# Kernel tuning notes

Measured on AMD Instinct MI355X. Metric: run time of the kernel, lower is better.

## Reference

```python
import jax, jax.numpy as jnp
import numpy as np

N, E, D, H = 50000, 800000, 64, 4  # nodes, edges, dim_h, heads
NEG_SLOPE = 0.2
BN_EPS = 1e-5


def setup_inputs() -> dict:
    key = jax.random.key(0)
    ks = jax.random.split(key, 8)
    x = jax.random.normal(ks[0], (N, D), dtype=jnp.float32)
    edge_index = jax.random.randint(ks[1], (2, E), 0, N, dtype=jnp.int32)
    s = 1.0 / np.sqrt(D)
    W_lin = jax.random.normal(ks[2], (D, D), dtype=jnp.float32) * s
    b_lin = jnp.zeros((D,), dtype=jnp.float32)
    prelu_w = jnp.full((D,), 0.25, dtype=jnp.float32)
    W_gat = jax.random.normal(ks[3], (H * D, D), dtype=jnp.float32) * s  # maps D -> H*D
    att_src = jax.random.normal(ks[4], (H, D), dtype=jnp.float32) * 0.1
    att_dst = jax.random.normal(ks[5], (H, D), dtype=jnp.float32) * 0.1
    gat_bias = jnp.zeros((D,), dtype=jnp.float32)
    bn_gamma = jnp.ones((D,), dtype=jnp.float32)
    bn_beta = jnp.zeros((D,), dtype=jnp.float32)
    return dict(x=x, edge_index=edge_index, W_lin=W_lin, b_lin=b_lin,
                prelu_w=prelu_w, W_gat=W_gat, att_src=att_src, att_dst=att_dst,
                gat_bias=gat_bias, bn_gamma=bn_gamma, bn_beta=bn_beta)


def _gat_mod_fwd(x, edge_index, W_lin, b_lin, prelu_w, W_gat, att_src, att_dst,
                 gat_bias, bn_gamma, bn_beta):
    # --- pre linear + PReLU ---
    x = x @ W_lin.T + b_lin
    x = jnp.where(x >= 0, x, prelu_w * x)  # per-channel PReLU

    # --- GATConv (concat=False -> head mean), add_self_loops=True ---
    h = (x @ W_gat.T).reshape(N, H, D)              # [N,H,D]
    a_src = jnp.einsum('nhd,hd->nh', h, att_src)    # [N,H]
    a_dst = jnp.einsum('nhd,hd->nh', h, att_dst)    # [N,H]

    loop = jnp.arange(N, dtype=edge_index.dtype)
    src = jnp.concatenate([edge_index[0], loop])    # [E+N]
    dst = jnp.concatenate([edge_index[1], loop])

    e = jax.nn.leaky_relu(a_src[src] + a_dst[dst], NEG_SLOPE)   # [E+N, H]
    # segment softmax over destination nodes (self loops guarantee non-empty)
    emax = jax.ops.segment_max(e, dst, num_segments=N)          # [N,H]
    p = jnp.exp(e - emax[dst])
    denom = jax.ops.segment_sum(p, dst, num_segments=N)         # [N,H]
    alpha = p / denom[dst]                                      # [E+N,H]

    msg = h[src] * alpha[:, :, None]                            # [E+N,H,D]
    out = jax.ops.segment_sum(msg, dst, num_segments=N)         # [N,H,D]
    out = out.mean(axis=1) + gat_bias                           # [N,D]

    # --- BatchNorm1d (training: batch stats) + ReLU ---
    mean = out.mean(axis=0)
    var = out.var(axis=0)
    out = bn_gamma * (out - mean) * jax.lax.rsqrt(var + BN_EPS) + bn_beta
    return jax.nn.relu(out)


def reference(x, edge_index, W_lin, b_lin, prelu_w, W_gat, att_src, att_dst,
              gat_bias, bn_gamma, bn_beta):
    return _gat_mod_fwd(x, edge_index, W_lin, b_lin, prelu_w, W_gat, att_src,
                        att_dst, gat_bias, bn_gamma, bn_beta)
```

## Files before the change

### kernel.cpp

```cpp
#include <hip/hip_runtime.h>
#include <hip/hip_fp16.h>

#define NEG_SLOPE 0.2f
#define BN_EPS 1e-5f

constexpr int D = 64;
constexpr int H = 4;

constexpr int PSORT = 128;
constexpr int MAXW2 = 12544;

typedef _Float16 half2_t __attribute__((ext_vector_type(2)));
typedef _Float16 half4_t __attribute__((ext_vector_type(4)));
typedef _Float16 half8_t __attribute__((ext_vector_type(8)));
typedef float f32x4_t __attribute__((ext_vector_type(4)));
typedef int i32x4 __attribute__((ext_vector_type(4)));

union Rec {
    i32x4 i4;
    struct { int idx; int pad; half4_t w; } f;
};

#define MFMA16(a, b, c) __builtin_amdgcn_mfma_f32_16x16x32_f16(a, b, c, 0, 0, 0)

#if __has_builtin(__builtin_amdgcn_fdot2)
#define FDOT2(a, b, c) __builtin_amdgcn_fdot2((a), (b), (c), false)
#else
#define FDOT2(a, b, c) ((c) + (float)(a)[0] * (float)(b)[0] + (float)(a)[1] * (float)(b)[1])
#endif

__device__ inline half2_t h2cast(unsigned int u) { return __builtin_bit_cast(half2_t, u); }

__device__ inline float lrelu(float v) { return (v >= 0.f) ? v : NEG_SLOPE * v; }

__device__ inline void split8(const float* p, bool ok, half8_t& hi, half8_t& lo) {
    float f[8];
    if (ok) {
        float4 a = *(const float4*)p;
        float4 b = *(const float4*)(p + 4);
        f[0] = a.x; f[1] = a.y; f[2] = a.z; f[3] = a.w;
        f[4] = b.x; f[5] = b.y; f[6] = b.z; f[7] = b.w;
    } else {
        #pragma unroll
        for (int j = 0; j < 8; j++) f[j] = 0.f;
    }
    #pragma unroll
    for (int j = 0; j < 8; j++) {
        _Float16 h = (_Float16)f[j];
        hi[j] = h;
        lo[j] = (_Float16)(f[j] - (float)h);
    }
}

__global__ __launch_bounds__(256) void k_node(
    const float* __restrict__ x,
    const float* __restrict__ W_lin, const float* __restrict__ b_lin,
    const float* __restrict__ prelu_w, const float* __restrict__ W_gat,
    const float* __restrict__ att_src, const float* __restrict__ att_dst,
    _Float16* __restrict__ hh, float* __restrict__ asrc_ws,
    float* __restrict__ adst_ws, int N)
{
    __shared__ _Float16 smem[32 * 264];
    _Float16* __restrict__ h_lds = smem;
    _Float16* __restrict__ x1hi  = smem;
    _Float16* __restrict__ x1lo  = smem + 32 * 72;

    const int t = threadIdx.x;
    const int w = t >> 6;
    const int l = t & 63;
    const int li = l & 15;
    const int lq = l >> 4;
    const int base = blockIdx.x * 32;
    const int nvalid = min(32, N - base);

    f32x4_t accA[2] = {};
    {
        half8_t blh[2], bll[2];
        const int n = 16 * w + li;
        #pragma unroll
        for (int ks = 0; ks < 2; ks++)
            split8(W_lin + n * 64 + 32 * ks + 8 * lq, true, blh[ks], bll[ks]);
        #pragma unroll
        for (int mt = 0; mt < 2; mt++) {
            const int row = base + 16 * mt + li;
            const bool ok = row < N;
            #pragma unroll
            for (int ks = 0; ks < 2; ks++) {
                half8_t ah, al;
                split8(x + (size_t)row * 64 + 32 * ks + 8 * lq, ok, ah, al);
                accA[mt] = MFMA16(ah, blh[ks], accA[mt]);
                accA[mt] = MFMA16(al, blh[ks], accA[mt]);
                accA[mt] = MFMA16(ah, bll[ks], accA[mt]);
            }
        }
    }

    {
        const int n = 16 * w + li;
        const float bl = b_lin[n];
        const float pw = prelu_w[n];
        #pragma unroll
        for (int mt = 0; mt < 2; mt++) {
            #pragma unroll
            for (int r = 0; r < 4; r++) {
                const int m = 16 * mt + lq * 4 + r;
                float v = accA[mt][r] + bl;
                v = (v >= 0.f) ? v : pw * v;
                _Float16 hi = (_Float16)v;
                x1hi[m * 72 + n] = hi;
                x1lo[m * 72 + n] = (_Float16)(v - (float)hi);
            }
        }
    }
    __syncthreads();

    half8_t xah[2][2], xal[2][2];
    #pragma unroll
    for (int mt = 0; mt < 2; mt++) {
        #pragma unroll
        for (int ks = 0; ks < 2; ks++) {
            const int off = (16 * mt + li) * 72 + 32 * ks + 8 * lq;
            xah[mt][ks] = *(const half8_t*)(&x1hi[off]);
            xal[mt][ks] = *(const half8_t*)(&x1lo[off]);
        }
    }
    f32x4_t accB[2][4] = {};
    #pragma unroll
    for (int nt = 0; nt < 4; nt++) {
        half8_t wh[2], wl[2];
        const int c = 64 * w + 16 * nt + li;
        #pragma unroll
        for (int ks = 0; ks < 2; ks++)
            split8(W_gat + (size_t)c * 64 + 32 * ks + 8 * lq, true, wh[ks], wl[ks]);
        #pragma unroll
        for (int mt = 0; mt < 2; mt++) {
            #pragma unroll
            for (int ks = 0; ks < 2; ks++) {
                accB[mt][nt] = MFMA16(xah[mt][ks], wh[ks], accB[mt][nt]);
                accB[mt][nt] = MFMA16(xal[mt][ks], wh[ks], accB[mt][nt]);
                accB[mt][nt] = MFMA16(xah[mt][ks], wl[ks], accB[mt][nt]);
            }
        }
    }

    {
        float asv[4], adv[4];
        #pragma unroll
        for (int nt = 0; nt < 4; nt++) {
            const int c = 64 * w + 16 * nt + li;
            asv[nt] = att_src[c];
            adv[nt] = att_dst[c];
        }
        #pragma unroll
        for (int mt = 0; mt < 2; mt++) {
            #pragma unroll
            for (int r = 0; r < 4; r++) {
                float s = 0.f, dsum = 0.f;
                #pragma unroll
                for (int nt = 0; nt < 4; nt++) {
                    s += accB[mt][nt][r] * asv[nt];
                    dsum += accB[mt][nt][r] * adv[nt];
                }
                #pragma unroll
                for (int off = 1; off < 16; off <<= 1) {
                    s += __shfl_xor(s, off, 64);
                    dsum += __shfl_xor(dsum, off, 64);
                }
                if (li == 0) {
                    const int m = 16 * mt + lq * 4 + r;
                    if (m < nvalid) {
                        asrc_ws[(size_t)(base + m) * H + w] = s;
                        adst_ws[(size_t)(base + m) * H + w] = dsum;
                    }
                }
            }
        }
    }

    __syncthreads();

    #pragma unroll
    for (int mt = 0; mt < 2; mt++) {
        #pragma unroll
        for (int nt = 0; nt < 4; nt++) {
            #pragma unroll
            for (int r = 0; r < 4; r++) {
                const int m = 16 * mt + lq * 4 + r;
                const int d = 16 * nt + li;
                h_lds[m * 264 + d * 4 + w] = (_Float16)accB[mt][nt][r];
            }
        }
    }
    __syncthreads();
    {
        const int chunks = nvalid * 32;
        const uint4* src = (const uint4*)h_lds;
        uint4* dst = (uint4*)(hh + (size_t)base * 256);
        for (int i = t; i < chunks; i += 256) {
            int row = i >> 5;
            int col = i & 31;
            dst[i] = src[row * 33 + col];
        }
    }
}

__global__ __launch_bounds__(1024) void k_hist(const int* __restrict__ ei,
                                               unsigned int* __restrict__ gcnt,
                                               int E, int chunk, int N2, int WTOT) {
    __shared__ unsigned int cnt[MAXW2];
    const int p = blockIdx.x & (PSORT - 1);
    const int pass = blockIdx.x >> 7;
    const int t = threadIdx.x;
    const int W2 = N2 >> 1;
    for (int i = t; i < W2; i += 1024) cnt[i] = 0;
    __syncthreads();
    const int e0 = p * chunk;
    const int e1 = min(E, e0 + chunk);
    const int nlo = pass * N2;
    for (int e = e0 + t; e < e1; e += 1024) {
        int dl = ei[E + e] - nlo;
        if ((unsigned)dl < (unsigned)N2)
            atomicAdd(&cnt[dl >> 1], 1u << ((dl & 1) * 16));
    }
    __syncthreads();
    unsigned int* dst = gcnt + (size_t)p * WTOT + (size_t)pass * W2;
    for (int i = t; i < W2; i += 1024) dst[i] = cnt[i];
}

__global__ __launch_bounds__(256) void k_off(unsigned int* __restrict__ gcnt,
                                             int* __restrict__ gcount,
                                             int* __restrict__ offs,
                                             int* __restrict__ deg,
                                             int N, int WTOT) {
    __shared__ int sm[256];
    __shared__ int sbase;
    const int t = threadIdx.x;
    const int i = blockIdx.x * 256 + t;
    int d0 = 0, d1 = 0;
    if (i < WTOT) {
        unsigned int run = 0;
        for (int p = 0; p < PSORT; p++) {
            unsigned int* q = gcnt + (size_t)p * WTOT + i;
            unsigned int c = *q;
            *q = run;
            run += c;
        }
        d0 = (int)(run & 0xffffu);
        d1 = (int)(run >> 16);
    }
    int v = d0 + d1;
    sm[t] = v;
    __syncthreads();
    for (int off = 1; off < 256; off <<= 1) {
        int u = (t >= off) ? sm[t - off] : 0;
        __syncthreads();
        sm[t] += u;
        __syncthreads();
    }
    if (t == 255) sbase = atomicAdd(gcount, sm[255]);
    __syncthreads();
    const int base = sbase + sm[t] - v;
    const int n0 = 2 * i;
    if (n0 < N)     { offs[n0] = base;          deg[n0] = d0; }
    if (n0 + 1 < N) { offs[n0 + 1] = base + d0; deg[n0 + 1] = d1; }
}

__global__ __launch_bounds__(1024) void k_fill(const int* __restrict__ ei,
                                               const unsigned int* __restrict__ gcnt,
                                               const int* __restrict__ offs,
                                               const float* __restrict__ asrc,
                                               const float* __restrict__ adst,
                                               i32x4* __restrict__ recs,
                                               int E, int chunk, int N2, int WTOT) {
    __shared__ unsigned int cur[MAXW2];
    const int p = blockIdx.x & (PSORT - 1);
    const int pass = blockIdx.x >> 7;
    const int t = threadIdx.x;
    const int W2 = N2 >> 1;
    for (int i = t; i < W2; i += 1024) cur[i] = 0;
    __syncthreads();
    const int e0 = p * chunk;
    const int e1 = min(E, e0 + chunk);
    const int nlo = pass * N2;
    for (int e = e0 + t; e < e1; e += 1024) {
        int d = ei[E + e];
        int dl = d - nlo;
        if ((unsigned)dl >= (unsigned)N2) continue;
        int s = ei[e];
        const unsigned int sh = (unsigned)(dl & 1) * 16;
        unsigned int old = atomicAdd(&cur[dl >> 1], 1u << sh);
        int lr = (int)((old >> sh) & 0xffffu);
        int pr = (int)((gcnt[(size_t)p * WTOT + (d >> 1)] >> sh) & 0xffffu);
        int pos = offs[d] + pr + lr;
        float4 a = *(const float4*)(asrc + (size_t)s * H);
        float4 b = *(const float4*)(adst + (size_t)d * H);
        Rec r;
        r.f.idx = s;
        r.f.pad = 0;
        r.f.w[0] = (_Float16)__expf(lrelu(a.x + b.x));
        r.f.w[1] = (_Float16)__expf(lrelu(a.y + b.y));
        r.f.w[2] = (_Float16)__expf(lrelu(a.z + b.z));
        r.f.w[3] = (_Float16)__expf(lrelu(a.w + b.w));
        recs[pos] = r.i4;
    }
}

__device__ inline void edge_pair(const i32x4 ra, const i32x4 rb,
                                 const uint2 ha, const uint2 hb,
                                 float& den0, float& den1, float& den2, float& den3,
                                 float& acc0, float& acc1, float& acc2, float& acc3)
{
    const half2_t one2 = h2cast(0x3C003C00u);
    unsigned int wp0 = __builtin_amdgcn_perm((unsigned int)rb.z, (unsigned int)ra.z, 0x05040100u);
    unsigned int wp1 = __builtin_amdgcn_perm((unsigned int)rb.z, (unsigned int)ra.z, 0x07060302u);
    unsigned int wp2 = __builtin_amdgcn_perm((unsigned int)rb.w, (unsigned int)ra.w, 0x05040100u);
    unsigned int wp3 = __builtin_amdgcn_perm((unsigned int)rb.w, (unsigned int)ra.w, 0x07060302u);
    unsigned int hp0 = __builtin_amdgcn_perm(hb.x, ha.x, 0x05040100u);
    unsigned int hp1 = __builtin_amdgcn_perm(hb.x, ha.x, 0x07060302u);
    unsigned int hp2 = __builtin_amdgcn_perm(hb.y, ha.y, 0x05040100u);
    unsigned int hp3 = __builtin_amdgcn_perm(hb.y, ha.y, 0x07060302u);
    den0 = FDOT2(h2cast(wp0), one2, den0);
    den1 = FDOT2(h2cast(wp1), one2, den1);
    den2 = FDOT2(h2cast(wp2), one2, den2);
    den3 = FDOT2(h2cast(wp3), one2, den3);
    acc0 = FDOT2(h2cast(wp0), h2cast(hp0), acc0);
    acc1 = FDOT2(h2cast(wp1), h2cast(hp1), acc1);
    acc2 = FDOT2(h2cast(wp2), h2cast(hp2), acc2);
    acc3 = FDOT2(h2cast(wp3), h2cast(hp3), acc3);
}

__global__ __launch_bounds__(256) void k_agg(
    const float* __restrict__ asrc, const float* __restrict__ adst,
    const int* __restrict__ offs, const int* __restrict__ deg,
    const i32x4* __restrict__ recs, const uint2* __restrict__ hh2,
    float* __restrict__ out, int N)
{
    int wid = (blockIdx.x * 256 + threadIdx.x) >> 6;
    int lane = threadIdx.x & 63;
    if (wid >= N) return;
    const int i = wid;

    float4 b = *(const float4*)(adst + (size_t)i * H);
    float4 a0 = *(const float4*)(asrc + (size_t)i * H);
    float ws0 = __expf(lrelu(a0.x + b.x));
    float ws1 = __expf(lrelu(a0.y + b.y));
    float ws2 = __expf(lrelu(a0.z + b.z));
    float ws3 = __expf(lrelu(a0.w + b.w));

    const int beg = __builtin_amdgcn_readfirstlane(offs[i]);
    const int dg  = __builtin_amdgcn_readfirstlane(deg[i]);

    float den0 = ws0, den1 = ws1, den2 = ws2, den3 = ws3;
    float acc0, acc1, acc2, acc3;
    {
        uint2 hv = hh2[(size_t)i * D + lane];
        half2_t s01 = h2cast(hv.x), s23 = h2cast(hv.y);
        acc0 = ws0 * (float)s01[0];
        acc1 = ws1 * (float)s01[1];
        acc2 = ws2 * (float)s23[0];
        acc3 = ws3 * (float)s23[1];
    }

    const int nfull = dg & ~7;
    int k = 0;
    for (; k < nfull; k += 8) {
        i32x4 rr[8];
        #pragma unroll
        for (int j = 0; j < 8; j++)
            rr[j] = __builtin_nontemporal_load(recs + beg + k + j);
        uint2 hv[8];
        #pragma unroll
        for (int j = 0; j < 8; j++)
            hv[j] = hh2[(size_t)rr[j].x * D + lane];
        #pragma unroll
        for (int j = 0; j < 8; j += 2)
            edge_pair(rr[j], rr[j + 1], hv[j], hv[j + 1],
                      den0, den1, den2, den3, acc0, acc1, acc2, acc3);
    }
    if (k < dg) {
        i32x4 rr[8];
        #pragma unroll
        for (int j = 0; j < 8; j++) {
            int kk = min(k + j, dg - 1);
            i32x4 r = __builtin_nontemporal_load(recs + beg + kk);
            if (k + j >= dg) { r.z = 0; r.w = 0; }
            rr[j] = r;
        }
        uint2 hv[8];
        #pragma unroll
        for (int j = 0; j < 8; j++)
            hv[j] = hh2[(size_t)rr[j].x * D + lane];
        #pragma unroll
        for (int j = 0; j < 8; j += 2)
            edge_pair(rr[j], rr[j + 1], hv[j], hv[j + 1],
                      den0, den1, den2, den3, acc0, acc1, acc2, acc3);
    }

    out[(size_t)i * D + lane] =
        0.25f * (acc0 / den0 + acc1 / den1 + acc2 / den2 + acc3 / den3);
}

__global__ __launch_bounds__(256) void k_bn_stats(const float* __restrict__ out,
                                                  float* __restrict__ sums,
                                                  int total) {
    const int t = threadIdx.x;
    const int stride = gridDim.x * 256;
    float s = 0.f, sq = 0.f;
    for (int idx = blockIdx.x * 256 + t; idx < total; idx += stride) {
        float v = out[idx];
        s += v;
        sq += v * v;
    }
    __shared__ float ls[256], lq[256];
    ls[t] = s;
    lq[t] = sq;
    __syncthreads();
    if (t < 64) {
        s = ls[t] + ls[t + 64] + ls[t + 128] + ls[t + 192];
        sq = lq[t] + lq[t + 64] + lq[t + 128] + lq[t + 192];
        atomicAdd(&sums[t], s);
        atomicAdd(&sums[64 + t], sq);
    }
}

__global__ __launch_bounds__(256) void k_bn_apply(float* __restrict__ out,
                                                  const float* __restrict__ sums,
                                                  const float* __restrict__ gamma,
                                                  const float* __restrict__ beta,
                                                  int total, float invN) {
    int idx = blockIdx.x * 256 + threadIdx.x;
    if (idx >= total) return;
    int c = idx & 63;
    float mean = sums[c] * invN;
    float var = sums[64 + c] * invN - mean * mean;
    float y = gamma[c] * (out[idx] - mean) * rsqrtf(var + BN_EPS) + beta[c];
    out[idx] = fmaxf(y, 0.f);
}

extern "C" void kernel_launch(void* const* d_in, const int* in_sizes, int n_in,
                              void* d_out, int out_size, void* d_ws, size_t ws_size,
                              hipStream_t stream) {
    const float* x       = (const float*)d_in[0];
    const int*   ei      = (const int*)d_in[1];
    const float* W_lin   = (const float*)d_in[2];
    const float* b_lin   = (const float*)d_in[3];
    const float* prelu_w = (const float*)d_in[4];
    const float* W_gat   = (const float*)d_in[5];
    const float* att_src = (const float*)d_in[6];
    const float* att_dst = (const float*)d_in[7];
    const float* bn_gamma = (const float*)d_in[9];
    const float* bn_beta  = (const float*)d_in[10];
    float* out = (float*)d_out;

    const int N = in_sizes[0] / D;
    const int E = in_sizes[1] / 2;

    int N2 = (N + 1) / 2;
    N2 = (N2 + 1) & ~1;
    const int WTOT = N2;
    const int chunk = (E + PSORT - 1) / PSORT;

    char* wp = (char*)d_ws;
    _Float16* hh = (_Float16*)wp;      wp += (size_t)N * D * H * sizeof(_Float16);
    float* asrc  = (float*)wp;          wp += (size_t)N * H * sizeof(float);
    float* adst  = (float*)wp;          wp += (size_t)N * H * sizeof(float);
    char* zero_base = wp;
    float* sums  = (float*)wp;          wp += 2 * D * sizeof(float);
    int* gcount  = (int*)wp;            wp += 4 * sizeof(int);
    size_t zero_bytes = (size_t)(wp - zero_base);
    int* offs    = (int*)wp;            wp += (size_t)((N + 3) & ~3) * sizeof(int);
    int* deg     = (int*)wp;            wp += (size_t)((N + 3) & ~3) * sizeof(int);
    i32x4* recs  = (i32x4*)wp;          wp += (size_t)E * sizeof(i32x4);
    unsigned int* gcnt;
    if ((size_t)PSORT * WTOT * sizeof(unsigned int) <= (size_t)out_size) {
        gcnt = (unsigned int*)d_out;
    } else {
        gcnt = (unsigned int*)wp;
        wp += (size_t)PSORT * WTOT * sizeof(unsigned int);
    }
    (void)ws_size; (void)n_in;

    const int total = N * D;
    const int NB1 = (N + 31) / 32;
    const int NBS = 2 * PSORT;
    const int NBO = (WTOT + 255) / 256;

    hipMemsetAsync(zero_base, 0, zero_bytes, stream);
    hipLaunchKernelGGL(k_node, dim3(NB1), dim3(256), 0, stream,
                       x, W_lin, b_lin, prelu_w, W_gat, att_src, att_dst,
                       hh, asrc, adst, N);
    hipLaunchKernelGGL(k_hist, dim3(NBS), dim3(1024), 0, stream,
                       ei, gcnt, E, chunk, N2, WTOT);
    hipLaunchKernelGGL(k_off, dim3(NBO), dim3(256), 0, stream,
                       gcnt, gcount, offs, deg, N, WTOT);
    hipLaunchKernelGGL(k_fill, dim3(NBS), dim3(1024), 0, stream,
                       ei, gcnt, offs, asrc, adst, recs, E, chunk, N2, WTOT);
    hipLaunchKernelGGL(k_agg, dim3((N + 3) / 4), dim3(256), 0, stream,
                       asrc, adst, offs, deg, recs, (const uint2*)hh, out, N);
    hipLaunchKernelGGL(k_bn_stats, dim3(1024), dim3(256), 0, stream,
                       out, sums, total);
    hipLaunchKernelGGL(k_bn_apply, dim3((total + 255) / 256), dim3(256), 0, stream,
                       out, sums, bn_gamma, bn_beta, total, 1.f / (float)N);
}
```

Measured before the change: 261.6 us.

## Record per-edge local rank in histogram pass and flatten the fill kernel

The histogram kernel now writes each edge's local rank, taken from the LDS atomic's old value, into a new rank buffer. The fill kernel becomes a flat one-thread-per-edge launch that no longer zeroes a shared-memory counter array or redoes the atomics. Edge chunks are fixed at 8192 per partition block so the fill kernel can find the partition with a shift. The offset kernel also loads 32 partition counts at a time to raise memory-level parallelism. The cost is an extra E-sized int buffer written and read, plus unbalanced histogram chunks, where some partition blocks are empty when E is well below 128*8192.

Result: faster. 246.3 us (-5.8%).

```diff
diff --git a/kernel.cpp b/kernel.cpp
--- a/kernel.cpp
+++ b/kernel.cpp
@@ -8,6 +8,8 @@
 constexpr int H = 4;
 
 constexpr int PSORT = 128;
+constexpr int CHUNK_SHIFT = 13;
+constexpr int CHUNK = 1 << CHUNK_SHIFT;
 constexpr int MAXW2 = 12544;
 
 typedef _Float16 half2_t __attribute__((ext_vector_type(2)));
@@ -206,7 +208,8 @@
 
 __global__ __launch_bounds__(1024) void k_hist(const int* __restrict__ ei,
                                                unsigned int* __restrict__ gcnt,
-                                               int E, int chunk, int N2, int WTOT) {
+                                               int* __restrict__ rank,
+                                               int E, int N2, int WTOT) {
     __shared__ unsigned int cnt[MAXW2];
     const int p = blockIdx.x & (PSORT - 1);
     const int pass = blockIdx.x >> 7;
@@ -214,13 +217,16 @@
     const int W2 = N2 >> 1;
     for (int i = t; i < W2; i += 1024) cnt[i] = 0;
     __syncthreads();
-    const int e0 = p * chunk;
-    const int e1 = min(E, e0 + chunk);
+    const int e0 = p << CHUNK_SHIFT;
+    const int e1 = min(E, e0 + CHUNK);
     const int nlo = pass * N2;
     for (int e = e0 + t; e < e1; e += 1024) {
         int dl = ei[E + e] - nlo;
-        if ((unsigned)dl < (unsigned)N2)
-            atomicAdd(&cnt[dl >> 1], 1u << ((dl & 1) * 16));
+        if ((unsigned)dl < (unsigned)N2) {
+            const unsigned int sh = (unsigned)(dl & 1) * 16;
+            unsigned int old = atomicAdd(&cnt[dl >> 1], 1u << sh);
+            rank[e] = (int)((old >> sh) & 0xffffu);
+        }
     }
     __syncthreads();
     unsigned int* dst = gcnt + (size_t)p * WTOT + (size_t)pass * W2;
@@ -239,11 +245,17 @@
     int d0 = 0, d1 = 0;
     if (i < WTOT) {
         unsigned int run = 0;
-        for (int p = 0; p < PSORT; p++) {
-            unsigned int* q = gcnt + (size_t)p * WTOT + i;
-            unsigned int c = *q;
-            *q = run;
-            run += c;
+        for (int pb = 0; pb < PSORT; pb += 32) {
+            unsigned int c[32];
+            #pragma unroll
+            for (int j = 0; j < 32; j++)
+                c[j] = gcnt[(size_t)(pb + j) * WTOT + i];
+            #pragma unroll
+            for (int j = 0; j < 32; j++) {
+                unsigned int cc = c[j];
+                gcnt[(size_t)(pb + j) * WTOT + i] = run;
+                run += cc;
+            }
         }
         d0 = (int)(run & 0xffffu);
         d1 = (int)(run >> 16);
@@ -265,44 +277,32 @@
     if (n0 + 1 < N) { offs[n0 + 1] = base + d0; deg[n0 + 1] = d1; }
 }
 
-__global__ __launch_bounds__(1024) void k_fill(const int* __restrict__ ei,
-                                               const unsigned int* __restrict__ gcnt,
-                                               const int* __restrict__ offs,
-                                               const float* __restrict__ asrc,
-                                               const float* __restrict__ adst,
-                                               i32x4* __restrict__ recs,
-                                               int E, int chunk, int N2, int WTOT) {
-    __shared__ unsigned int cur[MAXW2];
-    const int p = blockIdx.x & (PSORT - 1);
-    const int pass = blockIdx.x >> 7;
-    const int t = threadIdx.x;
-    const int W2 = N2 >> 1;
-    for (int i = t; i < W2; i += 1024) cur[i] = 0;
-    __syncthreads();
-    const int e0 = p * chunk;
-    const int e1 = min(E, e0 + chunk);
-    const int nlo = pass * N2;
-    for (int e = e0 + t; e < e1; e += 1024) {
-        int d = ei[E + e];
-        int dl = d - nlo;
-        if ((unsigned)dl >= (unsigned)N2) continue;
-        int s = ei[e];
-        const unsigned int sh = (unsigned)(dl & 1) * 16;
-        unsigned int old = atomicAdd(&cur[dl >> 1], 1u << sh);
-        int lr = (int)((old >> sh) & 0xffffu);
-        int pr = (int)((gcnt[(size_t)p * WTOT + (d >> 1)] >> sh) & 0xffffu);
-        int pos = offs[d] + pr + lr;
-        float4 a = *(const float4*)(asrc + (size_t)s * H);
-        float4 b = *(const float4*)(adst + (size_t)d * H);
-        Rec r;
-        r.f.idx = s;
-        r.f.pad = 0;
-        r.f.w[0] = (_Float16)__expf(lrelu(a.x + b.x));
-        r.f.w[1] = (_Float16)__expf(lrelu(a.y + b.y));
-        r.f.w[2] = (_Float16)__expf(lrelu(a.z + b.z));
-        r.f.w[3] = (_Float16)__expf(lrelu(a.w + b.w));
-        recs[pos] = r.i4;
-    }
+__global__ __launch_bounds__(256) void k_fill(const int* __restrict__ ei,
+                                              const unsigned int* __restrict__ gcnt,
+                                              const int* __restrict__ offs,
+                                              const int* __restrict__ rank,
+                                              const float* __restrict__ asrc,
+                                              const float* __restrict__ adst,
+                                              i32x4* __restrict__ recs,
+                                              int E, int WTOT) {
+    int e = blockIdx.x * 256 + threadIdx.x;
+    if (e >= E) return;
+    int s = ei[e];
+    int d = ei[E + e];
+    int p = e >> CHUNK_SHIFT;
+    const unsigned int sh = (unsigned)(d & 1) * 16;
+    int pr = (int)((gcnt[(size_t)p * WTOT + (d >> 1)] >> sh) & 0xffffu);
+    int pos = offs[d] + pr + rank[e];
+    float4 a = *(const float4*)(asrc + (size_t)s * H);
+    float4 b = *(const float4*)(adst + (size_t)d * H);
+    Rec r;
+    r.f.idx = s;
+    r.f.pad = 0;
+    r.f.w[0] = (_Float16)__expf(lrelu(a.x + b.x));
+    r.f.w[1] = (_Float16)__expf(lrelu(a.y + b.y));
+    r.f.w[2] = (_Float16)__expf(lrelu(a.z + b.z));
+    r.f.w[3] = (_Float16)__expf(lrelu(a.w + b.w));
+    recs[pos] = r.i4;
 }
 
 __device__ inline void edge_pair(const i32x4 ra, const i32x4 rb,
@@ -458,7 +458,6 @@
     int N2 = (N + 1) / 2;
     N2 = (N2 + 1) & ~1;
     const int WTOT = N2;
-    const int chunk = (E + PSORT - 1) / PSORT;
 
     char* wp = (char*)d_ws;
     _Float16* hh = (_Float16*)wp;      wp += (size_t)N * D * H * sizeof(_Float16);
@@ -470,6 +469,7 @@
     size_t zero_bytes = (size_t)(wp - zero_base);
     int* offs    = (int*)wp;            wp += (size_t)((N + 3) & ~3) * sizeof(int);
     int* deg     = (int*)wp;            wp += (size_t)((N + 3) & ~3) * sizeof(int);
+    int* rank    = (int*)wp;            wp += (size_t)((E + 3) & ~3) * sizeof(int);
     i32x4* recs  = (i32x4*)wp;          wp += (size_t)E * sizeof(i32x4);
     unsigned int* gcnt;
     if ((size_t)PSORT * WTOT * sizeof(unsigned int) <= (size_t)out_size) {
@@ -490,11 +490,11 @@
                        x, W_lin, b_lin, prelu_w, W_gat, att_src, att_dst,
                        hh, asrc, adst, N);
     hipLaunchKernelGGL(k_hist, dim3(NBS), dim3(1024), 0, stream,
-                       ei, gcnt, E, chunk, N2, WTOT);
+                       ei, gcnt, rank, E, N2, WTOT);
     hipLaunchKernelGGL(k_off, dim3(NBO), dim3(256), 0, stream,
                        gcnt, gcount, offs, deg, N, WTOT);
-    hipLaunchKernelGGL(k_fill, dim3(NBS), dim3(1024), 0, stream,
-                       ei, gcnt, offs, asrc, adst, recs, E, chunk, N2, WTOT);
+    hipLaunchKernelGGL(k_fill, dim3((E + 255) / 256), dim3(256), 0, stream,
+                       ei, gcnt, offs, rank, asrc, adst, recs, E, WTOT);
     hipLaunchKernelGGL(k_agg, dim3((N + 3) / 4), dim3(256), 0, stream,
                        asrc, adst, offs, deg, recs, (const uint2*)hh, out, N);
     hipLaunchKernelGGL(k_bn_stats, dim3(1024), dim3(256), 0, stream,
```
